# Kernel optimization log

Measured on AMD Instinct MI355X. Metric: run time of the kernel, lower is better.

Reference implementation:

```python
import jax, jax.numpy as jnp
import numpy as np

DEPTH, HEADS, DIM_HEAD = 6, 8, 64
B, N, E = 2, 128, 160
NUM_ATOMS, NF = 100, 127
DIM = NF + 1                 # 128, node feature dim fed to transformer
INNER = HEADS * DIM_HEAD     # 512


def setup_inputs() -> dict:
    key = jax.random.key(0)
    ks = iter(jax.random.split(key, 40))
    f32 = jnp.float32
    def w(shape, scale=0.02):
        return jax.random.normal(next(ks), shape, dtype=f32) * scale
    inp = {
        "indices": jax.random.randint(next(ks), (B, N), 0, NUM_ATOMS),
        "coordinates": jax.random.normal(next(ks), (B, N, 3), dtype=f32),
        "bonds": jax.random.randint(next(ks), (E, 2), 0, N),
        "noise_level": jax.random.uniform(next(ks), (1,), dtype=f32),
        "atom_emb": w((NUM_ATOMS, NF), 1.0),
        "ln1_g": jnp.ones((DEPTH, DIM), f32), "ln1_b": jnp.zeros((DEPTH, DIM), f32),
        "Wq": w((DEPTH, DIM, INNER)), "bq": jnp.zeros((DEPTH, INNER), f32),
        "Wkv": w((DEPTH, DIM, 2 * INNER)), "bkv": jnp.zeros((DEPTH, 2 * INNER), f32),
        "We": w((DEPTH, 3, INNER)), "be": jnp.zeros((DEPTH, INNER), f32),
        "Wo": w((DEPTH, INNER, DIM)), "bo": jnp.zeros((DEPTH, DIM), f32),
        "Wg1": w((DEPTH, 3 * DIM, 1)),
        "ln2_g": jnp.ones((DEPTH, DIM), f32), "ln2_b": jnp.zeros((DEPTH, DIM), f32),
        "W1": w((DEPTH, DIM, 4 * DIM)), "b1": jnp.zeros((DEPTH, 4 * DIM), f32),
        "W2": w((DEPTH, 4 * DIM, DIM)), "b2": jnp.zeros((DEPTH, DIM), f32),
        "Wg2": w((DEPTH, 3 * DIM, 1)),
        "Wlin": w((DIM, 1)), "blin": jnp.zeros((1,), f32),
    }
    return inp


def _ln(x, g, b, eps=1e-5):
    m = jnp.mean(x, -1, keepdims=True)
    v = jnp.mean((x - m) ** 2, -1, keepdims=True)
    return (x - m) * jax.lax.rsqrt(v + eps) * g + b


def _gated_residual(x, res, Wg):
    # gate = sigmoid(Linear([x, res, x-res])); out = x*gate + res*(1-gate)
    gate = jax.nn.sigmoid(jnp.concatenate([x, res, x - res], -1) @ Wg)  # (B,N,1)
    return x * gate + res * (1.0 - gate)


def _forward(indices, bonds, coordinates, noise_level, atom_emb,
             ln1_g, ln1_b, Wq, bq, Wkv, bkv, We, be, Wo, bo, Wg1,
             ln2_g, ln2_b, W1, b1, W2, b2, Wg2, Wlin, blin):
    b, n = indices.shape
    # nodes_embedding: atom embedding + noise-level channel
    noise = jnp.broadcast_to(noise_level.reshape(1, 1, 1).astype(coordinates.dtype), (b, n, 1))
    nodes = jnp.concatenate([atom_emb[indices], noise], -1)  # (B,N,DIM)
    # edges_embedding: vectorized scatter of per-bond coordinate differences
    i, j = bonds[:, 0], bonds[:, 1]
    diff = coordinates[:, i] - coordinates[:, j]             # (B,E,3)
    edges = jnp.zeros((b, n, n, 3), coordinates.dtype)
    edges = edges.at[:, i, j].set(diff).at[:, j, i].set(-diff)

    scale = DIM_HEAD ** -0.5
    for l in range(DEPTH):
        # PreNorm + edge-biased attention (mask is all-ones -> no-op)
        xn = _ln(nodes, ln1_g[l], ln1_b[l])
        q = (xn @ Wq[l] + bq[l]).reshape(b, n, HEADS, DIM_HEAD)
        k, v = jnp.split(xn @ Wkv[l] + bkv[l], 2, -1)
        k = k.reshape(b, n, HEADS, DIM_HEAD)
        v = v.reshape(b, n, HEADS, DIM_HEAD)
        e = (edges @ We[l] + be[l]).reshape(b, n, n, HEADS, DIM_HEAD)
        kk = k[:, None] + e                                   # (B,i,j,H,D)
        vv = v[:, None] + e
        sim = jnp.einsum('bihd,bijhd->bijh', q, kk) * scale
        attn = jax.nn.softmax(sim, axis=2)                    # softmax over j
        out = jnp.einsum('bijh,bijhd->bihd', attn, vv).reshape(b, n, INNER)
        out = out @ Wo[l] + bo[l]
        nodes = _gated_residual(out, nodes, Wg1[l])
        # PreNorm + FeedForward (exact GELU, mult=4) + gated residual
        xn = _ln(nodes, ln2_g[l], ln2_b[l])
        ff = jax.nn.gelu(xn @ W1[l] + b1[l], approximate=False) @ W2[l] + b2[l]
        nodes = _gated_residual(ff, nodes, Wg2[l])
    return jnp.sum(nodes @ Wlin + blin)


def reference(indices, coordinates, bonds, noise_level, atom_emb,
              ln1_g, ln1_b, Wq, bq, Wkv, bkv, We, be, Wo, bo, Wg1,
              ln2_g, ln2_b, W1, b1, W2, b2, Wg2, Wlin, blin):
    return _forward(indices, bonds, coordinates, noise_level, atom_emb,
                    ln1_g, ln1_b, Wq, bq, Wkv, bkv, We, be, Wo, bo, Wg1,
                    ln2_g, ln2_b, W1, b1, W2, b2, Wg2, Wlin, blin)
```

## Files before the change

kernel.cpp:

```cpp
#include <hip/hip_runtime.h>
#include <hip/hip_fp16.h>
#include <math.h>

#define DEPTH 6
#define HEADS 8
#define BB    2
#define NN    128
#define EE    160
#define NF    127
#define DIMM  128
#define INNER 512
#define NNODE 256

__device__ __forceinline__ void gload16(const void* g, void* l) {
    __builtin_amdgcn_global_load_lds((const __attribute__((address_space(1))) void*)g,
                                     (__attribute__((address_space(3))) void*)l,
                                     16, 0, 0);
}

__device__ __forceinline__ void wait_vm0() { __builtin_amdgcn_s_waitcnt(0x0f70); }
__device__ __forceinline__ void wait_lgkm0() { __builtin_amdgcn_s_waitcnt(0xC07F); }

__device__ __forceinline__ void wstage16(const char* gslice, char* ldsslice, int ln) {
#pragma unroll
    for (int i = 0; i < 16; i++)
        gload16(gslice + i * 1024 + ln * 16, ldsslice + i * 1024);
}
__device__ __forceinline__ void wstage16s(const char* gslice, int rowstride,
                                          char* ldsslice, int ln) {
#pragma unroll
    for (int i = 0; i < 16; i++)
        gload16(gslice + (size_t)i * rowstride + ln * 16, ldsslice + i * 1024);
}

__device__ __forceinline__ void fma8h(float4& a0, float4& a1, float s, float4 raw) {
    const __half2* hp = (const __half2*)&raw;
    float2 p0 = __half22float2(hp[0]), p1 = __half22float2(hp[1]);
    float2 p2 = __half22float2(hp[2]), p3 = __half22float2(hp[3]);
    a0.x += s * p0.x; a0.y += s * p0.y; a0.z += s * p1.x; a0.w += s * p1.y;
    a1.x += s * p2.x; a1.y += s * p2.y; a1.z += s * p3.x; a1.w += s * p3.y;
}

__device__ __forceinline__ void gemv512(const float* act, const float* wbuf,
                                        float* s_part, int w, int ln) {
    float4 a0 = {0,0,0,0}, a1 = {0,0,0,0};
    const float4* w4 = (const float4*)wbuf;
#pragma unroll
    for (int r = 0; r < 16; r++)
        fma8h(a0, a1, act[w * 16 + r], w4[r * 64 + ln]);
    ((float4*)(s_part + w * 512))[ln * 2]     = a0;
    ((float4*)(s_part + w * 512))[ln * 2 + 1] = a1;
}

__device__ __forceinline__ void gemv128(const float* act, const float* wbuf,
                                        float* s_part, int w, int ln) {
    float2 acc = {0, 0};
#pragma unroll 8
    for (int r = 0; r < 64; r++) {
        float raw = wbuf[r * 64 + ln];
        float2 p = __half22float2(*(const __half2*)&raw);
        float a = act[w * 64 + r];
        acc.x += a * p.x; acc.y += a * p.y;
    }
    s_part[w * 128 + ln * 2]     = acc.x;
    s_part[w * 128 + ln * 2 + 1] = acc.y;
}

template <int N>
__device__ __forceinline__ void block_reduce_n(float* vals, float* sbuf) {
#pragma unroll
    for (int off = 32; off > 0; off >>= 1)
#pragma unroll
        for (int q = 0; q < N; q++) vals[q] += __shfl_xor(vals[q], off, 64);
    int wave = threadIdx.x >> 6;
    if ((threadIdx.x & 63) == 0)
#pragma unroll
        for (int q = 0; q < N; q++) sbuf[wave * N + q] = vals[q];
    __syncthreads();
#pragma unroll
    for (int q = 0; q < N; q++) {
        float r = 0.0f;
#pragma unroll
        for (int g = 0; g < 8; g++) r += sbuf[g * N + q];
        vals[q] = r;
    }
    __syncthreads();
}

__device__ __forceinline__ float gelu_exact(float a) {
    return 0.5f * a * (1.0f + erff(a * 0.70710678f));
}


__global__ __launch_bounds__(512) void k_cvt(const float* Wq, const float* Wkv,
                                             const float* Wo, const float* W1,
                                             const float* W2,
                                             __half* hWq, __half* hWkv, __half* hWo,
                                             __half* hW1, __half* hW2,
                                             const float* blin, float* out) {
    if (blockIdx.x == 0 && threadIdx.x == 0) out[0] = 256.0f * blin[0];
    int g = blockIdx.x * 512 + threadIdx.x;
    const float4* src; __half* dst; int off;
    if (g < 98304)       { src = (const float4*)Wq;  dst = hWq;  off = g; }
    else if (g < 294912) { src = (const float4*)Wkv; dst = hWkv; off = g - 98304; }
    else if (g < 393216) { src = (const float4*)Wo;  dst = hWo;  off = g - 294912; }
    else if (g < 491520) { src = (const float4*)W1;  dst = hW1;  off = g - 393216; }
    else                 { src = (const float4*)W2;  dst = hW2;  off = g - 491520; }
    float4 v = src[off];
    __half2* d2 = (__half2*)(dst + (size_t)off * 4);
    d2[0] = __floats2half2_rn(v.x, v.y);
    d2[1] = __floats2half2_rn(v.z, v.w);
}

__global__ __launch_bounds__(512, 1) void k_pre(const int* indices, const float* noise,
                                                const float* atom_emb,
                                                const float* ln1_g, const float* ln1_b,
                                                const __half* hWq, const float* bq,
                                                const __half* hWkv, const float* bkv,
                                                float* nodes, float* qb,
                                                __half* hk, __half* hv) {
    int bn = blockIdx.x;
    int t  = threadIdx.x;
    int d  = t & 127;
    bool own = (t < 128);
    int w = t >> 6, ln = t & 63;
    __shared__ float arena[32768];
    __shared__ float s_xn[128];
    __shared__ float s_red[48];
    __shared__ float s_part[4096];
    char*  lslice = (char*)arena + w * 16384;
    float* wbuf   = arena + w * 4096;

    const char* WqL  = (const char*)hWq;
    const char* WkvL = (const char*)hWkv;
    wstage16(WqL + w * 16384, lslice, ln);

    float nd = 0.0f;
    if (own) {
        int idx = indices[bn];
        nd = (d < NF) ? atom_emb[idx * NF + d] : noise[0];
        nodes[bn * DIMM + d] = nd;
    }
    float vals[2] = {own ? nd : 0.0f, own ? nd * nd : 0.0f};
    block_reduce_n<2>(vals, s_red);
    float m   = vals[0] * (1.0f / 128.0f);
    float var = vals[1] * (1.0f / 128.0f) - m * m;
    if (own) s_xn[d] = (nd - m) * rsqrtf(var + 1e-5f) * ln1_g[d] + ln1_b[d];
    __syncthreads();

    wait_vm0();
    gemv512(s_xn, wbuf, s_part, w, ln);
    wait_lgkm0();
    wstage16s(WkvL + (size_t)(w * 16) * 2048, 2048, lslice, ln);
    __syncthreads();
    {
        float q = bq[t];
#pragma unroll
        for (int g = 0; g < 8; g++) q += s_part[g * 512 + t];
        qb[(size_t)bn * INNER + t] = q;
    }
    __syncthreads();

    wait_vm0();
    gemv512(s_xn, wbuf, s_part, w, ln);
    wait_lgkm0();
    wstage16s(WkvL + (size_t)(w * 16) * 2048 + 1024, 2048, lslice, ln);
    __syncthreads();
    {
        float k = bkv[t];
#pragma unroll
        for (int g = 0; g < 8; g++) k += s_part[g * 512 + t];
        hk[(size_t)bn * INNER + t] = __float2half(k);
    }
    __syncthreads();

    wait_vm0();
    gemv512(s_xn, wbuf, s_part, w, ln);
    __syncthreads();
    {
        float v = bkv[INNER + t];
#pragma unroll
        for (int g = 0; g < 8; g++) v += s_part[g * 512 + t];
        hv[(size_t)bn * INNER + t] = __float2half(v);
    }
}

__global__ __launch_bounds__(512, 1) void k_layer(int l,
        const float* coords, const int* bonds,
        const float* We, const float* be,
        float* qb, const __half* hkin, const __half* hvin,
        __half* hkout, __half* hvout,
        const __half* hWo, const float* bo, const float* Wg1,
        const float* ln2_g, const float* ln2_b,
        const __half* hW1, const float* b1,
        const __half* hW2, const float* b2,
        const float* Wg2,
        const float* ln1_g, const float* ln1_b,
        const __half* hWq, const float* bq,
        const __half* hWkv, const float* bkv,
        float* nodes, const float* Wlin, float* out) {
    int bn = blockIdx.x;
    int b = bn >> 7, i = bn & 127;
    int t = threadIdx.x;
    int d = t & 127;
    bool own = (t < 128);
    int w = t >> 6, ln = t & 63;

    __shared__ float arena[32768];
    __shared__ float scoord[384];
    __shared__ float sedge[384];
    __shared__ int   sadj[128];
    __shared__ float s_l[64];
    __shared__ float s_ao[512];
    __shared__ float s_h[512];
    __shared__ float s_xn[128];
    __shared__ float s_red[48];
    __shared__ float s_part[4096];
    float* s_o = s_part;
    char*  lslice = (char*)arena + w * 16384;
    float* wbuf   = arena + w * 4096;

    const char* WoL  = (const char*)(hWo + (size_t)l * INNER * DIMM);
    const char* W1L  = (const char*)(hW1 + (size_t)l * DIMM * 4 * DIMM);
    const char* W2L  = (const char*)(hW2 + (size_t)l * 4 * DIMM * DIMM);
    const char* WqL  = (const char*)(hWq + (size_t)(l + 1) * DIMM * INNER);
    const char* WkvL = (const char*)(hWkv + (size_t)(l + 1) * DIMM * 2 * INNER);

    wstage16(WoL + w * 16384, lslice, ln);

    const float4* qR4 = (const float4*)(qb + (size_t)bn * INNER);
    const float4* WeR = (const float4*)(We + (size_t)l * 3 * INNER);
    float4 qa  = qR4[ln * 2],        qz  = qR4[ln * 2 + 1];
    float4 w0a = WeR[ln * 2],        w0z = WeR[ln * 2 + 1];
    float4 w1a = WeR[128 + ln * 2],  w1z = WeR[129 + ln * 2];
    float4 w2a = WeR[256 + ln * 2],  w2z = WeR[257 + ln * 2];
    float4 bea = ((const float4*)(be + (size_t)l * INNER))[ln * 2];
    float4 bez = ((const float4*)(be + (size_t)l * INNER))[ln * 2 + 1];
    float res = own ? nodes[bn * DIMM + d] : 0.0f;

    if (t < 3 * NN) scoord[t] = coords[b * 3 * NN + t];
    if (t < NN) sadj[t] = 0;
    __syncthreads();
    if (t < EE) {
        int e0 = bonds[2 * t], e1 = bonds[2 * t + 1];
        if (e0 == i) sadj[e1] = 1;
        if (e1 == i) sadj[e0] = 1;
    }
    __syncthreads();
    if (t < NN) {
        int j = t;
        float msk = sadj[j] ? 1.0f : 0.0f;
        sedge[3 * j + 0] = msk * (scoord[3 * i + 0] - scoord[3 * j + 0]);
        sedge[3 * j + 1] = msk * (scoord[3 * i + 1] - scoord[3 * j + 1]);
        sedge[3 * j + 2] = msk * (scoord[3 * i + 2] - scoord[3 * j + 2]);
    }
    __syncthreads();

    const float4* kR = (const float4*)(hkin + (size_t)b * NN * INNER);
    const float4* vR = (const float4*)(hvin + (size_t)b * NN * INNER);
    float l_run = 0.0f;
    float4 o0 = {0, 0, 0, 0}, o1 = {0, 0, 0, 0};
    int j0 = w * 16;
#pragma unroll
    for (int base = 0; base < 16; base += 4) {
        float4 kraw[4], vraw[4];
#pragma unroll
        for (int p = 0; p < 4; p++) {
            int j = j0 + base + p;
            kraw[p] = kR[j * 64 + ln];
            vraw[p] = vR[j * 64 + ln];
        }
#pragma unroll
        for (int p = 0; p < 4; p++) {
            int j = j0 + base + p;
            float ex = sedge[3 * j], ey = sedge[3 * j + 1], ez = sedge[3 * j + 2];
            float4 e0, e1;
            e0.x = bea.x + ex * w0a.x + ey * w1a.x + ez * w2a.x;
            e0.y = bea.y + ex * w0a.y + ey * w1a.y + ez * w2a.y;
            e0.z = bea.z + ex * w0a.z + ey * w1a.z + ez * w2a.z;
            e0.w = bea.w + ex * w0a.w + ey * w1a.w + ez * w2a.w;
            e1.x = bez.x + ex * w0z.x + ey * w1z.x + ez * w2z.x;
            e1.y = bez.y + ex * w0z.y + ey * w1z.y + ez * w2z.y;
            e1.z = bez.z + ex * w0z.z + ey * w1z.z + ez * w2z.z;
            e1.w = bez.w + ex * w0z.w + ey * w1z.w + ez * w2z.w;
            const __half2* kh = (const __half2*)&kraw[p];
            float2 k0 = __half22float2(kh[0]), k1 = __half22float2(kh[1]);
            float2 k2 = __half22float2(kh[2]), k3 = __half22float2(kh[3]);
            float s = qa.x * (k0.x + e0.x) + qa.y * (k0.y + e0.y)
                    + qa.z * (k1.x + e0.z) + qa.w * (k1.y + e0.w)
                    + qz.x * (k2.x + e1.x) + qz.y * (k2.y + e1.y)
                    + qz.z * (k3.x + e1.z) + qz.w * (k3.y + e1.w);
            s += __shfl_xor(s, 1, 64);
            s += __shfl_xor(s, 2, 64);
            s += __shfl_xor(s, 4, 64);
            float pp = __expf(s * 0.125f);
            const __half2* vh = (const __half2*)&vraw[p];
            float2 v0 = __half22float2(vh[0]), v1 = __half22float2(vh[1]);
            float2 v2 = __half22float2(vh[2]), v3 = __half22float2(vh[3]);
            l_run += pp;
            o0.x += pp * (v0.x + e0.x); o0.y += pp * (v0.y + e0.y);
            o0.z += pp * (v1.x + e0.z); o0.w += pp * (v1.y + e0.w);
            o1.x += pp * (v2.x + e1.x); o1.y += pp * (v2.y + e1.y);
            o1.z += pp * (v3.x + e1.z); o1.w += pp * (v3.y + e1.w);
        }
    }
    ((float4*)(s_o + w * 512))[ln * 2]     = o0;
    ((float4*)(s_o + w * 512))[ln * 2 + 1] = o1;
    if ((ln & 7) == 0) s_l[w * 8 + (ln >> 3)] = l_run;
    __syncthreads();
    {
        float o = 0.0f;
#pragma unroll
        for (int g = 0; g < 8; g++) o += s_o[g * 512 + t];
        int h = t >> 6;
        float lsum = 0.0f;
#pragma unroll
        for (int g = 0; g < 8; g++) lsum += s_l[g * 8 + h];
        s_ao[t] = o / lsum;
    }
    __syncthreads();

    wait_vm0();
    gemv128(s_ao, wbuf, s_part, w, ln);
    wait_lgkm0();
    wstage16(W1L + w * 16384, lslice, ln);
    __syncthreads();
    float x = 0.0f;
    if (own) {
        x = bo[l * DIMM + d];
#pragma unroll
        for (int g = 0; g < 8; g++) x += s_part[g * 128 + d];
    }

    const float* Wg1_l = Wg1 + l * 3 * DIMM;
    float n1;
    {
        float tex = own ? (x * Wg1_l[d] + res * Wg1_l[DIMM + d] + (x - res) * Wg1_l[2 * DIMM + d]) : 0.0f;
        float vals[6] = {tex,
                         own ? x : 0.0f, own ? x * x : 0.0f,
                         own ? x * res : 0.0f,
                         own ? res : 0.0f, own ? res * res : 0.0f};
        block_reduce_n<6>(vals, s_red);
        float g1 = 1.0f / (1.0f + __expf(-vals[0]));
        float sn  = g1 * vals[1] + (1.0f - g1) * vals[4];
        float sn2 = g1 * g1 * vals[2] + 2.0f * g1 * (1.0f - g1) * vals[3]
                  + (1.0f - g1) * (1.0f - g1) * vals[5];
        float m   = sn * (1.0f / 128.0f);
        float var = sn2 * (1.0f / 128.0f) - m * m;
        n1 = x * g1 + res * (1.0f - g1);
        if (own) s_xn[d] = (n1 - m) * rsqrtf(var + 1e-5f) * ln2_g[l * DIMM + d] + ln2_b[l * DIMM + d];
    }
    __syncthreads();

    wait_vm0();
    gemv512(s_xn, wbuf, s_part, w, ln);
    wait_lgkm0();
    wstage16(W2L + w * 16384, lslice, ln);
    __syncthreads();
    {
        float a = b1[l * 4 * DIMM + t];
#pragma unroll
        for (int g = 0; g < 8; g++) a += s_part[g * 512 + t];
        s_h[t] = gelu_exact(a);
    }
    __syncthreads();

    wait_vm0();
    gemv128(s_h, wbuf, s_part, w, ln);
    wait_lgkm0();
    if (l < DEPTH - 1) wstage16(WqL + w * 16384, lslice, ln);
    __syncthreads();
    float y = 0.0f;
    if (own) {
        y = b2[l * DIMM + d];
#pragma unroll
        for (int g = 0; g < 8; g++) y += s_part[g * 128 + d];
    }

    const float* Wg2_l = Wg2 + l * 3 * DIMM;
    if (l < DEPTH - 1) {
        float tex = own ? (y * Wg2_l[d] + n1 * Wg2_l[DIMM + d] + (y - n1) * Wg2_l[2 * DIMM + d]) : 0.0f;
        float vals[6] = {tex,
                         own ? y : 0.0f, own ? y * y : 0.0f,
                         own ? y * n1 : 0.0f,
                         own ? n1 : 0.0f, own ? n1 * n1 : 0.0f};
        block_reduce_n<6>(vals, s_red);
        float g2 = 1.0f / (1.0f + __expf(-vals[0]));
        float sn  = g2 * vals[1] + (1.0f - g2) * vals[4];
        float sn2 = g2 * g2 * vals[2] + 2.0f * g2 * (1.0f - g2) * vals[3]
                  + (1.0f - g2) * (1.0f - g2) * vals[5];
        float m   = sn * (1.0f / 128.0f);
        float var = sn2 * (1.0f / 128.0f) - m * m;
        float n2 = y * g2 + n1 * (1.0f - g2);
        if (own) {
            nodes[bn * DIMM + d] = n2;
            s_xn[d] = (n2 - m) * rsqrtf(var + 1e-5f) * ln1_g[(l + 1) * DIMM + d]
                    + ln1_b[(l + 1) * DIMM + d];
        }
        __syncthreads();

        wait_vm0();
        gemv512(s_xn, wbuf, s_part, w, ln);
        wait_lgkm0();
        wstage16s(WkvL + (size_t)(w * 16) * 2048, 2048, lslice, ln);
        __syncthreads();
        {
            float q = bq[(l + 1) * INNER + t];
#pragma unroll
            for (int g = 0; g < 8; g++) q += s_part[g * 512 + t];
            qb[(size_t)bn * INNER + t] = q;
        }
        __syncthreads();

        wait_vm0();
        gemv512(s_xn, wbuf, s_part, w, ln);
        wait_lgkm0();
        wstage16s(WkvL + (size_t)(w * 16) * 2048 + 1024, 2048, lslice, ln);
        __syncthreads();
        {
            float k = bkv[(l + 1) * 2 * INNER + t];
#pragma unroll
            for (int g = 0; g < 8; g++) k += s_part[g * 512 + t];
            hkout[(size_t)bn * INNER + t] = __float2half(k);
        }
        __syncthreads();

        wait_vm0();
        gemv512(s_xn, wbuf, s_part, w, ln);
        __syncthreads();
        {
            float v = bkv[(l + 1) * 2 * INNER + INNER + t];
#pragma unroll
            for (int g = 0; g < 8; g++) v += s_part[g * 512 + t];
            hvout[(size_t)bn * INNER + t] = __float2half(v);
        }
    } else {
        float wl = own ? Wlin[d] : 0.0f;
        float tex = own ? (y * Wg2_l[d] + n1 * Wg2_l[DIMM + d] + (y - n1) * Wg2_l[2 * DIMM + d]) : 0.0f;
        float vals[3] = {tex, y * wl, n1 * wl};
        block_reduce_n<3>(vals, s_red);
        float g2 = 1.0f / (1.0f + __expf(-vals[0]));
        float tot = g2 * vals[1] + (1.0f - g2) * vals[2];
        if (t == 0) atomicAdd(out, tot);
    }
}

extern "C" void kernel_launch(void* const* d_in, const int* in_sizes, int n_in,
                              void* d_out, int out_size, void* d_ws, size_t ws_size,
                              hipStream_t stream) {
    const int*   indices = (const int*)d_in[0];
    const float* coords  = (const float*)d_in[1];
    const int*   bonds   = (const int*)d_in[2];
    const float* noise   = (const float*)d_in[3];
    const float* atom_emb= (const float*)d_in[4];
    const float* ln1_g   = (const float*)d_in[5];
    const float* ln1_b   = (const float*)d_in[6];
    const float* Wq      = (const float*)d_in[7];
    const float* bq      = (const float*)d_in[8];
    const float* Wkv     = (const float*)d_in[9];
    const float* bkv     = (const float*)d_in[10];
    const float* We      = (const float*)d_in[11];
    const float* be      = (const float*)d_in[12];
    const float* Wo      = (const float*)d_in[13];
    const float* bo      = (const float*)d_in[14];
    const float* Wg1     = (const float*)d_in[15];
    const float* ln2_g   = (const float*)d_in[16];
    const float* ln2_b   = (const float*)d_in[17];
    const float* W1      = (const float*)d_in[18];
    const float* b1      = (const float*)d_in[19];
    const float* W2      = (const float*)d_in[20];
    const float* b2      = (const float*)d_in[21];
    const float* Wg2     = (const float*)d_in[22];
    const float* Wlin    = (const float*)d_in[23];
    const float* blin    = (const float*)d_in[24];

    float*  ws    = (float*)d_ws;
    float*  nodes = ws;
    float*  qb    = nodes + NNODE * DIMM;
    __half* hkb   = (__half*)(qb + NNODE * INNER);
    __half* hvb   = hkb + 2 * NNODE * INNER;
    __half* hWq   = hvb + 2 * NNODE * INNER;
    __half* hWkv  = hWq + DEPTH * DIMM * INNER;
    __half* hWo   = hWkv + DEPTH * DIMM * 2 * INNER;
    __half* hW1   = hWo + DEPTH * INNER * DIMM;
    __half* hW2   = hW1 + DEPTH * DIMM * 4 * DIMM;

    k_cvt<<<1152, 512, 0, stream>>>(Wq, Wkv, Wo, W1, W2, hWq, hWkv, hWo, hW1, hW2,
                                    blin, (float*)d_out);
    k_pre<<<NNODE, 512, 0, stream>>>(indices, noise, atom_emb, ln1_g, ln1_b,
                                     hWq, bq, hWkv, bkv, nodes, qb, hkb, hvb);
    for (int l = 0; l < DEPTH; l++) {
        const __half* hkin = hkb + (size_t)(l & 1) * NNODE * INNER;
        const __half* hvin = hvb + (size_t)(l & 1) * NNODE * INNER;
        __half* hkout = hkb + (size_t)((l + 1) & 1) * NNODE * INNER;
        __half* hvout = hvb + (size_t)((l + 1) & 1) * NNODE * INNER;
        k_layer<<<NNODE, 512, 0, stream>>>(l, coords, bonds, We, be,
                                           qb, hkin, hvin, hkout, hvout,
                                           hWo, bo, Wg1, ln2_g, ln2_b, hW1, b1, hW2, b2,
                                           Wg2, ln1_g, ln1_b, hWq, bq, hWkv, bkv,
                                           nodes, Wlin, (float*)d_out);
    }
}
```

Before: 270.1 us.

## Split weight staging into halves and skip edge math for unbonded pairs

Weight staging into LDS is split into two 8-row halves, so the next matrix's first half is prefetched while the second half of the current GEMV is still computing. This overlaps global-to-LDS loads with compute instead of serializing them. The attention loop now computes q·k with packed fp16 dot instructions. It applies the edge-embedding term only for bonded pairs, using a precomputed q·bias constant and a summed bias contribution for unbonded ones. This reduces per-pair ALU work, but rounding q to fp16 before the dot product lowers precision.

```diff
diff --git a/kernel.cpp b/kernel.cpp
--- a/kernel.cpp
+++ b/kernel.cpp
@@ -12,24 +12,39 @@
 #define INNER 512
 #define NNODE 256
 
+typedef _Float16 h2f16 __attribute__((ext_vector_type(2)));
+
+#if defined(__has_builtin)
+#if __has_builtin(__builtin_amdgcn_fdot2)
+#define HAVE_FDOT2 1
+#endif
+#endif
+
+__device__ __forceinline__ float fdot2f(h2f16 a, h2f16 b, float c) {
+#ifdef HAVE_FDOT2
+    return __builtin_amdgcn_fdot2(a, b, c, false);
+#else
+    return c + (float)a.x * (float)b.x + (float)a.y * (float)b.y;
+#endif
+}
+
 __device__ __forceinline__ void gload16(const void* g, void* l) {
     __builtin_amdgcn_global_load_lds((const __attribute__((address_space(1))) void*)g,
                                      (__attribute__((address_space(3))) void*)l,
                                      16, 0, 0);
 }
 
-__device__ __forceinline__ void wait_vm0() { __builtin_amdgcn_s_waitcnt(0x0f70); }
+template <int N>
+__device__ __forceinline__ void wait_vm() {
+    __builtin_amdgcn_s_waitcnt((0xF << 8) | (7 << 4) | (N & 0xF) | ((N >> 4) << 14));
+}
 __device__ __forceinline__ void wait_lgkm0() { __builtin_amdgcn_s_waitcnt(0xC07F); }
-
-__device__ __forceinline__ void wstage16(const char* gslice, char* ldsslice, int ln) {
-#pragma unroll
-    for (int i = 0; i < 16; i++)
-        gload16(gslice + i * 1024 + ln * 16, ldsslice + i * 1024);
-}
-__device__ __forceinline__ void wstage16s(const char* gslice, int rowstride,
-                                          char* ldsslice, int ln) {
-#pragma unroll
-    for (int i = 0; i < 16; i++)
+__device__ __forceinline__ void sbar0() { __builtin_amdgcn_sched_barrier(0); }
+
+__device__ __forceinline__ void stage8s(const char* gslice, int rowstride,
+                                        char* ldsslice, int ln) {
+#pragma unroll
+    for (int i = 0; i < 8; i++)
         gload16(gslice + (size_t)i * rowstride + ln * 16, ldsslice + i * 1024);
 }
 
@@ -41,27 +56,53 @@
     a1.x += s * p2.x; a1.y += s * p2.y; a1.z += s * p3.x; a1.w += s * p3.y;
 }
 
-__device__ __forceinline__ void gemv512(const float* act, const float* wbuf,
-                                        float* s_part, int w, int ln) {
+__device__ __forceinline__ void gemv512_pipe(const float* act, float* wbuf,
+                                             float* s_part,
+                                             const char* nextA, const char* nextB,
+                                             int nextStride, int w, int ln) {
     float4 a0 = {0,0,0,0}, a1 = {0,0,0,0};
     const float4* w4 = (const float4*)wbuf;
-#pragma unroll
-    for (int r = 0; r < 16; r++)
+    wait_vm<8>();
+#pragma unroll
+    for (int r = 0; r < 8; r++)
         fma8h(a0, a1, act[w * 16 + r], w4[r * 64 + ln]);
+    wait_lgkm0(); sbar0();
+    if (nextA) { stage8s(nextA, nextStride, (char*)wbuf, ln); wait_vm<8>(); }
+    else       { wait_vm<0>(); }
+#pragma unroll
+    for (int r = 8; r < 16; r++)
+        fma8h(a0, a1, act[w * 16 + r], w4[r * 64 + ln]);
+    wait_lgkm0(); sbar0();
+    if (nextB) stage8s(nextB, nextStride, (char*)wbuf + 8192, ln);
     ((float4*)(s_part + w * 512))[ln * 2]     = a0;
     ((float4*)(s_part + w * 512))[ln * 2 + 1] = a1;
 }
 
-__device__ __forceinline__ void gemv128(const float* act, const float* wbuf,
-                                        float* s_part, int w, int ln) {
+__device__ __forceinline__ void gemv128_pipe(const float* act, float* wbuf,
+                                             float* s_part,
+                                             const char* nextA, const char* nextB,
+                                             int nextStride, int w, int ln) {
     float2 acc = {0, 0};
+    wait_vm<8>();
 #pragma unroll 8
-    for (int r = 0; r < 64; r++) {
+    for (int r = 0; r < 32; r++) {
         float raw = wbuf[r * 64 + ln];
         float2 p = __half22float2(*(const __half2*)&raw);
         float a = act[w * 64 + r];
         acc.x += a * p.x; acc.y += a * p.y;
     }
+    wait_lgkm0(); sbar0();
+    if (nextA) { stage8s(nextA, nextStride, (char*)wbuf, ln); wait_vm<8>(); }
+    else       { wait_vm<0>(); }
+#pragma unroll 8
+    for (int r = 32; r < 64; r++) {
+        float raw = wbuf[r * 64 + ln];
+        float2 p = __half22float2(*(const __half2*)&raw);
+        float a = act[w * 64 + r];
+        acc.x += a * p.x; acc.y += a * p.y;
+    }
+    wait_lgkm0(); sbar0();
+    if (nextB) stage8s(nextB, nextStride, (char*)wbuf + 8192, ln);
     s_part[w * 128 + ln * 2]     = acc.x;
     s_part[w * 128 + ln * 2 + 1] = acc.y;
 }
@@ -133,7 +174,8 @@
 
     const char* WqL  = (const char*)hWq;
     const char* WkvL = (const char*)hWkv;
-    wstage16(WqL + w * 16384, lslice, ln);
+    stage8s(WqL + w * 16384, 1024, lslice, ln);
+    stage8s(WqL + w * 16384 + 8192, 1024, lslice + 8192, ln);
 
     float nd = 0.0f;
     if (own) {
@@ -148,10 +190,9 @@
     if (own) s_xn[d] = (nd - m) * rsqrtf(var + 1e-5f) * ln1_g[d] + ln1_b[d];
     __syncthreads();
 
-    wait_vm0();
-    gemv512(s_xn, wbuf, s_part, w, ln);
-    wait_lgkm0();
-    wstage16s(WkvL + (size_t)(w * 16) * 2048, 2048, lslice, ln);
+    gemv512_pipe(s_xn, wbuf, s_part,
+                 WkvL + (size_t)(w * 16) * 2048,
+                 WkvL + (size_t)(w * 16 + 8) * 2048, 2048, w, ln);
     __syncthreads();
     {
         float q = bq[t];
@@ -161,10 +202,9 @@
     }
     __syncthreads();
 
-    wait_vm0();
-    gemv512(s_xn, wbuf, s_part, w, ln);
-    wait_lgkm0();
-    wstage16s(WkvL + (size_t)(w * 16) * 2048 + 1024, 2048, lslice, ln);
+    gemv512_pipe(s_xn, wbuf, s_part,
+                 WkvL + (size_t)(w * 16) * 2048 + 1024,
+                 WkvL + (size_t)(w * 16 + 8) * 2048 + 1024, 2048, w, ln);
     __syncthreads();
     {
         float k = bkv[t];
@@ -174,8 +214,7 @@
     }
     __syncthreads();
 
-    wait_vm0();
-    gemv512(s_xn, wbuf, s_part, w, ln);
+    gemv512_pipe(s_xn, wbuf, s_part, nullptr, nullptr, 0, w, ln);
     __syncthreads();
     {
         float v = bkv[INNER + t];
@@ -226,7 +265,8 @@
     const char* WqL  = (const char*)(hWq + (size_t)(l + 1) * DIMM * INNER);
     const char* WkvL = (const char*)(hWkv + (size_t)(l + 1) * DIMM * 2 * INNER);
 
-    wstage16(WoL + w * 16384, lslice, ln);
+    stage8s(WoL + w * 16384, 1024, lslice, ln);
+    stage8s(WoL + w * 16384 + 8192, 1024, lslice + 8192, ln);
 
     const float4* qR4 = (const float4*)(qb + (size_t)bn * INNER);
     const float4* WeR = (const float4*)(We + (size_t)l * 3 * INNER);
@@ -237,6 +277,13 @@
     float4 bea = ((const float4*)(be + (size_t)l * INNER))[ln * 2];
     float4 bez = ((const float4*)(be + (size_t)l * INNER))[ln * 2 + 1];
     float res = own ? nodes[bn * DIMM + d] : 0.0f;
+    h2f16 qh0 = {(_Float16)qa.x, (_Float16)qa.y};
+    h2f16 qh1 = {(_Float16)qa.z, (_Float16)qa.w};
+    h2f16 qh2 = {(_Float16)qz.x, (_Float16)qz.y};
+    h2f16 qh3 = {(_Float16)qz.z, (_Float16)qz.w};
+    float c = qa.x * bea.x + qa.y * bea.y + qa.z * bea.z + qa.w * bea.w
+            + qz.x * bez.x + qz.y * bez.y + qz.z * bez.z + qz.w * bez.w;
+    c += __shfl_xor(c, 1, 64); c += __shfl_xor(c, 2, 64); c += __shfl_xor(c, 4, 64);
 
     if (t < 3 * NN) scoord[t] = coords[b * 3 * NN + t];
     if (t < NN) sadj[t] = 0;
@@ -258,7 +305,7 @@
 
     const float4* kR = (const float4*)(hkin + (size_t)b * NN * INNER);
     const float4* vR = (const float4*)(hvin + (size_t)b * NN * INNER);
-    float l_run = 0.0f;
+    float l_run = 0.0f, S_nb = 0.0f;
     float4 o0 = {0, 0, 0, 0}, o1 = {0, 0, 0, 0};
     int j0 = w * 16;
 #pragma unroll
@@ -273,37 +320,45 @@
 #pragma unroll
         for (int p = 0; p < 4; p++) {
             int j = j0 + base + p;
-            float ex = sedge[3 * j], ey = sedge[3 * j + 1], ez = sedge[3 * j + 2];
+            const h2f16* kh = (const h2f16*)&kraw[p];
+            float s = fdot2f(qh0, kh[0],
+                      fdot2f(qh1, kh[1],
+                      fdot2f(qh2, kh[2],
+                      fdot2f(qh3, kh[3], 0.0f))));
+            bool bonded = (sadj[j] != 0);
             float4 e0, e1;
-            e0.x = bea.x + ex * w0a.x + ey * w1a.x + ez * w2a.x;
-            e0.y = bea.y + ex * w0a.y + ey * w1a.y + ez * w2a.y;
-            e0.z = bea.z + ex * w0a.z + ey * w1a.z + ez * w2a.z;
-            e0.w = bea.w + ex * w0a.w + ey * w1a.w + ez * w2a.w;
-            e1.x = bez.x + ex * w0z.x + ey * w1z.x + ez * w2z.x;
-            e1.y = bez.y + ex * w0z.y + ey * w1z.y + ez * w2z.y;
-            e1.z = bez.z + ex * w0z.z + ey * w1z.z + ez * w2z.z;
-            e1.w = bez.w + ex * w0z.w + ey * w1z.w + ez * w2z.w;
-            const __half2* kh = (const __half2*)&kraw[p];
-            float2 k0 = __half22float2(kh[0]), k1 = __half22float2(kh[1]);
-            float2 k2 = __half22float2(kh[2]), k3 = __half22float2(kh[3]);
-            float s = qa.x * (k0.x + e0.x) + qa.y * (k0.y + e0.y)
-                    + qa.z * (k1.x + e0.z) + qa.w * (k1.y + e0.w)
-                    + qz.x * (k2.x + e1.x) + qz.y * (k2.y + e1.y)
-                    + qz.z * (k3.x + e1.z) + qz.w * (k3.y + e1.w);
+            if (bonded) {
+                float ex = sedge[3 * j], ey = sedge[3 * j + 1], ez = sedge[3 * j + 2];
+                e0.x = bea.x + ex * w0a.x + ey * w1a.x + ez * w2a.x;
+                e0.y = bea.y + ex * w0a.y + ey * w1a.y + ez * w2a.y;
+                e0.z = bea.z + ex * w0a.z + ey * w1a.z + ez * w2a.z;
+                e0.w = bea.w + ex * w0a.w + ey * w1a.w + ez * w2a.w;
+                e1.x = bez.x + ex * w0z.x + ey * w1z.x + ez * w2z.x;
+                e1.y = bez.y + ex * w0z.y + ey * w1z.y + ez * w2z.y;
+                e1.z = bez.z + ex * w0z.z + ey * w1z.z + ez * w2z.z;
+                e1.w = bez.w + ex * w0z.w + ey * w1z.w + ez * w2z.w;
+                s += qa.x * e0.x + qa.y * e0.y + qa.z * e0.z + qa.w * e0.w
+                   + qz.x * e1.x + qz.y * e1.y + qz.z * e1.z + qz.w * e1.w;
+            }
             s += __shfl_xor(s, 1, 64);
             s += __shfl_xor(s, 2, 64);
             s += __shfl_xor(s, 4, 64);
+            if (!bonded) s += c;
             float pp = __expf(s * 0.125f);
+            l_run += pp;
             const __half2* vh = (const __half2*)&vraw[p];
             float2 v0 = __half22float2(vh[0]), v1 = __half22float2(vh[1]);
             float2 v2 = __half22float2(vh[2]), v3 = __half22float2(vh[3]);
-            l_run += pp;
-            o0.x += pp * (v0.x + e0.x); o0.y += pp * (v0.y + e0.y);
-            o0.z += pp * (v1.x + e0.z); o0.w += pp * (v1.y + e0.w);
-            o1.x += pp * (v2.x + e1.x); o1.y += pp * (v2.y + e1.y);
-            o1.z += pp * (v3.x + e1.z); o1.w += pp * (v3.y + e1.w);
+            o0.x += pp * v0.x; o0.y += pp * v0.y; o0.z += pp * v1.x; o0.w += pp * v1.y;
+            o1.x += pp * v2.x; o1.y += pp * v2.y; o1.z += pp * v3.x; o1.w += pp * v3.y;
+            if (bonded) {
+                o0.x += pp * e0.x; o0.y += pp * e0.y; o0.z += pp * e0.z; o0.w += pp * e0.w;
+                o1.x += pp * e1.x; o1.y += pp * e1.y; o1.z += pp * e1.z; o1.w += pp * e1.w;
+            } else S_nb += pp;
         }
     }
+    o0.x += S_nb * bea.x; o0.y += S_nb * bea.y; o0.z += S_nb * bea.z; o0.w += S_nb * bea.w;
+    o1.x += S_nb * bez.x; o1.y += S_nb * bez.y; o1.z += S_nb * bez.z; o1.w += S_nb * bez.w;
     ((float4*)(s_o + w * 512))[ln * 2]     = o0;
     ((float4*)(s_o + w * 512))[ln * 2 + 1] = o1;
     if ((ln & 7) == 0) s_l[w * 8 + (ln >> 3)] = l_run;
@@ -320,10 +375,8 @@
     }
     __syncthreads();
 
-    wait_vm0();
-    gemv128(s_ao, wbuf, s_part, w, ln);
-    wait_lgkm0();
-    wstage16(W1L + w * 16384, lslice, ln);
+    gemv128_pipe(s_ao, wbuf, s_part,
+                 W1L + w * 16384, W1L + w * 16384 + 8192, 1024, w, ln);
     __syncthreads();
     float x = 0.0f;
     if (own) {
@@ -335,7 +388,8 @@
     const float* Wg1_l = Wg1 + l * 3 * DIMM;
     float n1;
     {
-        float tex = own ? (x * Wg1_l[d] + res * Wg1_l[DIMM + d] + (x - res) * Wg1_l[2 * DIMM + d]) : 0.0f;
+        float tex = own ? (x * Wg1_l[d] + res * Wg1_l[DIMM + d]
+                           + (x - res) * Wg1_l[2 * DIMM + d]) : 0.0f;
         float vals[6] = {tex,
                          own ? x : 0.0f, own ? x * x : 0.0f,
                          own ? x * res : 0.0f,
@@ -348,14 +402,13 @@
         float m   = sn * (1.0f / 128.0f);
         float var = sn2 * (1.0f / 128.0f) - m * m;
         n1 = x * g1 + res * (1.0f - g1);
-        if (own) s_xn[d] = (n1 - m) * rsqrtf(var + 1e-5f) * ln2_g[l * DIMM + d] + ln2_b[l * DIMM + d];
-    }
-    __syncthreads();
-
-    wait_vm0();
-    gemv512(s_xn, wbuf, s_part, w, ln);
-    wait_lgkm0();
-    wstage16(W2L + w * 16384, lslice, ln);
+        if (own) s_xn[d] = (n1 - m) * rsqrtf(var + 1e-5f) * ln2_g[l * DIMM + d]
+                         + ln2_b[l * DIMM + d];
+    }
+    __syncthreads();
+
+    gemv512_pipe(s_xn, wbuf, s_part,
+                 W2L + w * 16384, W2L + w * 16384 + 8192, 1024, w, ln);
     __syncthreads();
     {
         float a = b1[l * 4 * DIMM + t];
@@ -365,10 +418,9 @@
     }
     __syncthreads();
 
-    wait_vm0();
-    gemv128(s_h, wbuf, s_part, w, ln);
-    wait_lgkm0();
-    if (l < DEPTH - 1) wstage16(WqL + w * 16384, lslice, ln);
+    gemv128_pipe(s_h, wbuf, s_part,
+                 (l < DEPTH - 1) ? WqL + w * 16384 : nullptr,
+                 (l < DEPTH - 1) ? WqL + w * 16384 + 8192 : nullptr, 1024, w, ln);
     __syncthreads();
     float y = 0.0f;
     if (own) {
@@ -379,7 +431,8 @@
 
     const float* Wg2_l = Wg2 + l * 3 * DIMM;
     if (l < DEPTH - 1) {
-        float tex = own ? (y * Wg2_l[d] + n1 * Wg2_l[DIMM + d] + (y - n1) * Wg2_l[2 * DIMM + d]) : 0.0f;
+        float tex = own ? (y * Wg2_l[d] + n1 * Wg2_l[DIMM + d]
+                           + (y - n1) * Wg2_l[2 * DIMM + d]) : 0.0f;
         float vals[6] = {tex,
                          own ? y : 0.0f, own ? y * y : 0.0f,
                          own ? y * n1 : 0.0f,
@@ -399,10 +452,9 @@
         }
         __syncthreads();
 
-        wait_vm0();
-        gemv512(s_xn, wbuf, s_part, w, ln);
-        wait_lgkm0();
-        wstage16s(WkvL + (size_t)(w * 16) * 2048, 2048, lslice, ln);
+        gemv512_pipe(s_xn, wbuf, s_part,
+                     WkvL + (size_t)(w * 16) * 2048,
+                     WkvL + (size_t)(w * 16 + 8) * 2048, 2048, w, ln);
         __syncthreads();
         {
             float q = bq[(l + 1) * INNER + t];
@@ -412,10 +464,9 @@
         }
         __syncthreads();
 
-        wait_vm0();
-        gemv512(s_xn, wbuf, s_part, w, ln);
-        wait_lgkm0();
-        wstage16s(WkvL + (size_t)(w * 16) * 2048 + 1024, 2048, lslice, ln);
+        gemv512_pipe(s_xn, wbuf, s_part,
+                     WkvL + (size_t)(w * 16) * 2048 + 1024,
+                     WkvL + (size_t)(w * 16 + 8) * 2048 + 1024, 2048, w, ln);
         __syncthreads();
         {
             float k = bkv[(l + 1) * 2 * INNER + t];
@@ -425,8 +476,7 @@
         }
         __syncthreads();
 
-        wait_vm0();
-        gemv512(s_xn, wbuf, s_part, w, ln);
+        gemv512_pipe(s_xn, wbuf, s_part, nullptr, nullptr, 0, w, ln);
         __syncthreads();
         {
             float v = bkv[(l + 1) * 2 * INNER + INNER + t];
@@ -436,7 +486,8 @@
         }
     } else {
         float wl = own ? Wlin[d] : 0.0f;
-        float tex = own ? (y * Wg2_l[d] + n1 * Wg2_l[DIMM + d] + (y - n1) * Wg2_l[2 * DIMM + d]) : 0.0f;
+        float tex = own ? (y * Wg2_l[d] + n1 * Wg2_l[DIMM + d]
+                           + (y - n1) * Wg2_l[2 * DIMM + d]) : 0.0f;
         float vals[3] = {tex, y * wl, n1 * wl};
         block_reduce_n<3>(vals, s_red);
         float g2 = 1.0f / (1.0f + __expf(-vals[0]));
```

After: 259.6 us. 3.9% less time.
